# Kernel tuning notes

Hardware: AMD Instinct MI355X
Metric: run time of the kernel (lower is better)

## Reference

```python
import jax, jax.numpy as jnp
import numpy as np

IN_FEATURES = 128
HIDDEN_DIM = 128
ALPHA = 0.2
NEG_INF = -9e15


def setup_inputs() -> dict:
    key = jax.random.key(0)
    k1, k2, k3, k4, k5 = jax.random.split(key, 5)
    N, n_context = 20000, 32
    h_i = jax.random.normal(k1, (N, IN_FEATURES), dtype=jnp.float32)
    context_indices = jax.random.randint(k2, (N, n_context), 0, N, dtype=jnp.int64)
    # learned params (torch nn.Linear default init scale ~ U(-1/sqrt(fan_in), 1/sqrt(fan_in)))
    s1 = 1.0 / np.sqrt(IN_FEATURES)
    s2 = 1.0 / np.sqrt(2 * HIDDEN_DIM)
    W_i = jax.random.uniform(k3, (IN_FEATURES, HIDDEN_DIM), jnp.float32, -s1, s1)
    W_j = jax.random.uniform(k4, (IN_FEATURES, HIDDEN_DIM), jnp.float32, -s1, s1)
    ka, kb = jax.random.split(k5)
    a_w = jax.random.uniform(ka, (2 * HIDDEN_DIM, 1), jnp.float32, -s2, s2)
    a_b = jax.random.uniform(kb, (1,), jnp.float32, -s2, s2)
    return {"h_i": h_i, "context_indices": context_indices,
            "W_i": W_i, "W_j": W_j, "a_w": a_w, "a_b": a_b}


def reference(h_i, context_indices, W_i, W_j, a_w, a_b):
    N, n_context = context_indices.shape
    # -1 padding maps to an extra zero row (torch indexes -1 -> last row of padded table)
    h_padded = jnp.concatenate([h_i, jnp.zeros((1, h_i.shape[1]), h_i.dtype)], axis=0)
    idx = jnp.where(context_indices >= 0, context_indices, N)
    h_j = h_padded[idx]                      # [N, n_context, in_features]
    Wh_i = h_i @ W_i                         # [N, hidden]
    Wh_j = jnp.einsum('ncf,fh->nch', h_j, W_j)  # [N, n_context, hidden]
    # attention_layer(cat(Wh_i, Wh_j)) split into two matvecs (same math as concat)
    a_i, a_j = a_w[:HIDDEN_DIM, 0], a_w[HIDDEN_DIM:, 0]
    e = Wh_i @ a_i                           # [N]
    e = e[:, None] + Wh_j @ a_j + a_b[0]     # [N, n_context]
    e = jax.nn.leaky_relu(e, ALPHA)
    e = jnp.where(context_indices >= 0, e, NEG_INF)
    attn = jax.nn.softmax(e, axis=1)         # [N, n_context]
    h_prime = jnp.einsum('nc,nch->nh', attn, Wh_j)
    return h_prime
```

## Files before the change

kernel.cpp:

```cpp
#include <hip/hip_runtime.h>
#include <hip/hip_fp16.h>

#define GAT_ALPHA 0.2f
#define GAT_NEG_INF -9.0e15f

__global__ void gat_precompute_vi(const float* __restrict__ Wi,
                                  const float* __restrict__ aw,
                                  float* __restrict__ vi) {
    int f = threadIdx.x;
    float s = 0.f;
    #pragma unroll 8
    for (int h = 0; h < 128; ++h)
        s = fmaf(Wi[f * 128 + h], aw[h], s);
    vi[f] = s;
}

__global__ __launch_bounds__(256) void gat_transform(
    const float* __restrict__ h, const float* __restrict__ Wj,
    const float* __restrict__ aw, const float* __restrict__ ab,
    const float* __restrict__ vi,
    __half* __restrict__ Wh16, float* __restrict__ e1, float* __restrict__ e2,
    int N) {
    __shared__ float4 sW[128 * 32];
    const float4* Wj4 = (const float4*)Wj;
    int t = threadIdx.x;
    #pragma unroll
    for (int i = 0; i < 16; ++i) sW[t + i * 256] = Wj4[t + i * 256];
    __syncthreads();

    const int wave = t >> 6, lane = t & 63, half = lane >> 5, l32 = lane & 31;
    const float abv = ab[0];
    const float4 viv = ((const float4*)vi)[l32];
    const float4 ajv = ((const float4*)(aw + 128))[l32];
    const float4* h4 = (const float4*)h;
    const int npairs = (N + 1) >> 1;

    for (int pair = blockIdx.x * 4 + wave; pair < npairs; pair += gridDim.x * 4) {
        int n = 2 * pair + half;
        bool ok = (n < N);
        int nc = ok ? n : 0;
        const float4* hrow = h4 + (size_t)nc * 32;
        float4 hreg = hrow[l32];
        float ax = 0.f, ay = 0.f, az = 0.f, aw4 = 0.f;
        #pragma unroll 4
        for (int fb = 0; fb < 32; ++fb) {
            float4 hq = hrow[fb];
            float4 w0 = sW[(4 * fb + 0) * 32 + l32];
            float4 w1 = sW[(4 * fb + 1) * 32 + l32];
            float4 w2 = sW[(4 * fb + 2) * 32 + l32];
            float4 w3 = sW[(4 * fb + 3) * 32 + l32];
            ax = fmaf(hq.x, w0.x, ax); ay = fmaf(hq.x, w0.y, ay);
            az = fmaf(hq.x, w0.z, az); aw4 = fmaf(hq.x, w0.w, aw4);
            ax = fmaf(hq.y, w1.x, ax); ay = fmaf(hq.y, w1.y, ay);
            az = fmaf(hq.y, w1.z, az); aw4 = fmaf(hq.y, w1.w, aw4);
            ax = fmaf(hq.z, w2.x, ax); ay = fmaf(hq.z, w2.y, ay);
            az = fmaf(hq.z, w2.z, az); aw4 = fmaf(hq.z, w2.w, aw4);
            ax = fmaf(hq.w, w3.x, ax); ay = fmaf(hq.w, w3.y, ay);
            az = fmaf(hq.w, w3.z, az); aw4 = fmaf(hq.w, w3.w, aw4);
        }
        if (ok) {
            union { __half hh[4]; float2 f2; } u;
            u.hh[0] = __float2half(ax); u.hh[1] = __float2half(ay);
            u.hh[2] = __float2half(az); u.hh[3] = __float2half(aw4);
            *(float2*)(Wh16 + (size_t)n * 128 + 4 * l32) = u.f2;
            float pe2 = ax * ajv.x + ay * ajv.y + az * ajv.z + aw4 * ajv.w;
            float pe1 = hreg.x * viv.x + hreg.y * viv.y + hreg.z * viv.z + hreg.w * viv.w;
            #pragma unroll
            for (int mm = 1; mm < 32; mm <<= 1) {
                pe2 += __shfl_xor(pe2, mm);
                pe1 += __shfl_xor(pe1, mm);
            }
            if (l32 == 0) { e2[n] = pe2; e1[n] = pe1 + abv; }
        }
    }
}

__global__ __launch_bounds__(256) void gat_gather(
    const int* __restrict__ ctx, const float* __restrict__ e1,
    const float* __restrict__ e2, const __half* __restrict__ Wh16,
    float* __restrict__ out, int N) {
    int t = threadIdx.x;
    int wave = t >> 6, lane = t & 63, c = lane & 31;
    for (int n = blockIdx.x * 4 + wave; n < N; n += gridDim.x * 4) {
        int iv = ctx[n * 32 + c];
        bool valid = iv >= 0;
        int j = valid ? iv : 0;
        float lg = e1[n] + e2[j];
        lg = fmaxf(lg, GAT_ALPHA * lg);
        lg = valid ? lg : GAT_NEG_INF;
        float m = lg;
        #pragma unroll
        for (int s = 16; s; s >>= 1) m = fmaxf(m, __shfl_xor(m, s));
        float p = valid ? __expf(lg - m) : 0.f;
        float ssum = p;
        #pragma unroll
        for (int s = 16; s; s >>= 1) ssum += __shfl_xor(ssum, s);
        p = (ssum > 0.f) ? p / ssum : 0.f;
        float a0 = 0.f, a1 = 0.f;
        #pragma unroll 16
        for (int cc = 0; cc < 32; ++cc) {
            float w = __shfl(p, cc);
            int jj = __shfl(j, cc);
            __half2 hv = *((const __half2*)(Wh16 + (size_t)jj * 128) + lane);
            float2 f2 = __half22float2(hv);
            a0 = fmaf(w, f2.x, a0);
            a1 = fmaf(w, f2.y, a1);
        }
        ((float2*)(out + (size_t)n * 128))[lane] = make_float2(a0, a1);
    }
}

extern "C" void kernel_launch(void* const* d_in, const int* in_sizes, int n_in,
                              void* d_out, int out_size, void* d_ws, size_t ws_size,
                              hipStream_t stream) {
    const float* h   = (const float*)d_in[0];
    const int*   ctx = (const int*)d_in[1];
    const float* Wi  = (const float*)d_in[2];
    const float* Wj  = (const float*)d_in[3];
    const float* aw  = (const float*)d_in[4];
    const float* ab  = (const float*)d_in[5];
    float* out = (float*)d_out;
    const int N = in_sizes[0] / 128;

    float* vi = (float*)d_ws;
    float* e1 = vi + 256;
    float* e2 = e1 + N;
    __half* Wh16 = (__half*)(e2 + N);

    gat_precompute_vi<<<1, 128, 0, stream>>>(Wi, aw, vi);
    gat_transform<<<512, 256, 0, stream>>>(h, Wj, aw, ab, vi, Wh16, e1, e2, N);
    gat_gather<<<(N + 3) / 4, 256, 0, stream>>>(ctx, e1, e2, Wh16, out, N);
}
```

Before: 110.4 us.

## Use MFMA fp16 for the transform and pack two nodes per wave in gather

The transform kernel is rewritten to run the h·W_j product on 16x16x32 fp16 MFMA instructions, reading a transposed, padded fp16 copy of W_j from shared memory. Each wave now handles 16-row tiles and uses a grid capped at 160 blocks. The gather kernel is rewritten so each wave processes two nodes with 32 lanes each, and each lane loads four halves per neighbour instead of two. The aim is to cut FMA-bound transform time and raise gather efficiency, at the cost of fp16 rounding of inputs and weights in the matmul and scattered 2-byte stores of Wh16.

```diff
diff --git a/kernel.cpp b/kernel.cpp
--- a/kernel.cpp
+++ b/kernel.cpp
@@ -3,6 +3,10 @@
 
 #define GAT_ALPHA 0.2f
 #define GAT_NEG_INF -9.0e15f
+
+typedef _Float16 half8_t __attribute__((ext_vector_type(8)));
+typedef _Float16 half4_t __attribute__((ext_vector_type(4)));
+typedef float f32x4 __attribute__((ext_vector_type(4)));
 
 __global__ void gat_precompute_vi(const float* __restrict__ Wi,
                                   const float* __restrict__ aw,
@@ -15,98 +19,155 @@
     vi[f] = s;
 }
 
-__global__ __launch_bounds__(256) void gat_transform(
+__global__ __launch_bounds__(256) void gat_transform_mfma(
     const float* __restrict__ h, const float* __restrict__ Wj,
     const float* __restrict__ aw, const float* __restrict__ ab,
     const float* __restrict__ vi,
     __half* __restrict__ Wh16, float* __restrict__ e1, float* __restrict__ e2,
     int N) {
-    __shared__ float4 sW[128 * 32];
-    const float4* Wj4 = (const float4*)Wj;
-    int t = threadIdx.x;
-    #pragma unroll
-    for (int i = 0; i < 16; ++i) sW[t + i * 256] = Wj4[t + i * 256];
+    __shared__ _Float16 sWt[128 * 136];
+    const int t = threadIdx.x;
+    for (int i = t; i < 128 * 128; i += 256) {
+        int k = i >> 7, n = i & 127;
+        sWt[n * 136 + k] = (_Float16)Wj[i];
+    }
     __syncthreads();
 
-    const int wave = t >> 6, lane = t & 63, half = lane >> 5, l32 = lane & 31;
+    const int wave = t >> 6, lane = t & 63, q = lane >> 4, l16 = lane & 15;
     const float abv = ab[0];
-    const float4 viv = ((const float4*)vi)[l32];
-    const float4 ajv = ((const float4*)(aw + 128))[l32];
-    const float4* h4 = (const float4*)h;
-    const int npairs = (N + 1) >> 1;
 
-    for (int pair = blockIdx.x * 4 + wave; pair < npairs; pair += gridDim.x * 4) {
-        int n = 2 * pair + half;
-        bool ok = (n < N);
-        int nc = ok ? n : 0;
-        const float4* hrow = h4 + (size_t)nc * 32;
-        float4 hreg = hrow[l32];
-        float ax = 0.f, ay = 0.f, az = 0.f, aw4 = 0.f;
-        #pragma unroll 4
-        for (int fb = 0; fb < 32; ++fb) {
-            float4 hq = hrow[fb];
-            float4 w0 = sW[(4 * fb + 0) * 32 + l32];
-            float4 w1 = sW[(4 * fb + 1) * 32 + l32];
-            float4 w2 = sW[(4 * fb + 2) * 32 + l32];
-            float4 w3 = sW[(4 * fb + 3) * 32 + l32];
-            ax = fmaf(hq.x, w0.x, ax); ay = fmaf(hq.x, w0.y, ay);
-            az = fmaf(hq.x, w0.z, az); aw4 = fmaf(hq.x, w0.w, aw4);
-            ax = fmaf(hq.y, w1.x, ax); ay = fmaf(hq.y, w1.y, ay);
-            az = fmaf(hq.y, w1.z, az); aw4 = fmaf(hq.y, w1.w, aw4);
-            ax = fmaf(hq.z, w2.x, ax); ay = fmaf(hq.z, w2.y, ay);
-            az = fmaf(hq.z, w2.z, az); aw4 = fmaf(hq.z, w2.w, aw4);
-            ax = fmaf(hq.w, w3.x, ax); ay = fmaf(hq.w, w3.y, ay);
-            az = fmaf(hq.w, w3.z, az); aw4 = fmaf(hq.w, w3.w, aw4);
+    float vir[4][8];
+    {
+        const float4* vi4 = (const float4*)vi;
+        #pragma unroll
+        for (int s = 0; s < 4; ++s) {
+            float4 u0 = vi4[s * 8 + q * 2];
+            float4 u1 = vi4[s * 8 + q * 2 + 1];
+            vir[s][0] = u0.x; vir[s][1] = u0.y; vir[s][2] = u0.z; vir[s][3] = u0.w;
+            vir[s][4] = u1.x; vir[s][5] = u1.y; vir[s][6] = u1.z; vir[s][7] = u1.w;
         }
-        if (ok) {
-            union { __half hh[4]; float2 f2; } u;
-            u.hh[0] = __float2half(ax); u.hh[1] = __float2half(ay);
-            u.hh[2] = __float2half(az); u.hh[3] = __float2half(aw4);
-            *(float2*)(Wh16 + (size_t)n * 128 + 4 * l32) = u.f2;
-            float pe2 = ax * ajv.x + ay * ajv.y + az * ajv.z + aw4 * ajv.w;
-            float pe1 = hreg.x * viv.x + hreg.y * viv.y + hreg.z * viv.z + hreg.w * viv.w;
+    }
+    float ajr[8];
+    #pragma unroll
+    for (int c = 0; c < 8; ++c) ajr[c] = aw[128 + c * 16 + l16];
+
+    const int ntiles = (N + 15) >> 4;
+    for (int tile = blockIdx.x * 4 + wave; tile < ntiles; tile += gridDim.x * 4) {
+        const int base = tile << 4;
+        int row = base + l16; if (row >= N) row = N - 1;
+        const float* hp = h + (size_t)row * 128 + q * 8;
+
+        half8_t af[4];
+        float pe1 = 0.f;
+        #pragma unroll
+        for (int s = 0; s < 4; ++s) {
+            float4 f0 = *(const float4*)(hp + s * 32);
+            float4 f1 = *(const float4*)(hp + s * 32 + 4);
+            pe1 = fmaf(f0.x, vir[s][0], pe1); pe1 = fmaf(f0.y, vir[s][1], pe1);
+            pe1 = fmaf(f0.z, vir[s][2], pe1); pe1 = fmaf(f0.w, vir[s][3], pe1);
+            pe1 = fmaf(f1.x, vir[s][4], pe1); pe1 = fmaf(f1.y, vir[s][5], pe1);
+            pe1 = fmaf(f1.z, vir[s][6], pe1); pe1 = fmaf(f1.w, vir[s][7], pe1);
+            half8_t a;
+            a[0] = (_Float16)f0.x; a[1] = (_Float16)f0.y;
+            a[2] = (_Float16)f0.z; a[3] = (_Float16)f0.w;
+            a[4] = (_Float16)f1.x; a[5] = (_Float16)f1.y;
+            a[6] = (_Float16)f1.z; a[7] = (_Float16)f1.w;
+            af[s] = a;
+        }
+
+        f32x4 acc[8];
+        #pragma unroll
+        for (int c = 0; c < 8; ++c) { f32x4 z = {0.f, 0.f, 0.f, 0.f}; acc[c] = z; }
+
+        const _Float16* wbase = sWt + l16 * 136 + q * 8;
+        #pragma unroll
+        for (int s = 0; s < 4; ++s) {
             #pragma unroll
-            for (int mm = 1; mm < 32; mm <<= 1) {
-                pe2 += __shfl_xor(pe2, mm);
-                pe1 += __shfl_xor(pe1, mm);
+            for (int c = 0; c < 8; ++c) {
+                half8_t bf = *(const half8_t*)(wbase + c * (16 * 136) + s * 32);
+                acc[c] = __builtin_amdgcn_mfma_f32_16x16x32_f16(af[s], bf, acc[c], 0, 0, 0);
             }
-            if (l32 == 0) { e2[n] = pe2; e1[n] = pe1 + abv; }
+        }
+
+        const bool full = (base + 16 <= N);
+        float pe2[4] = {0.f, 0.f, 0.f, 0.f};
+        #pragma unroll
+        for (int c = 0; c < 8; ++c) {
+            #pragma unroll
+            for (int r = 0; r < 4; ++r) {
+                float v = acc[c][r];
+                pe2[r] = fmaf(v, ajr[c], pe2[r]);
+                int rr = base + q * 4 + r;
+                if (full || rr < N)
+                    Wh16[(size_t)rr * 128 + (c * 16 + l16)] = __float2half(v);
+            }
+        }
+        #pragma unroll
+        for (int r = 0; r < 4; ++r) {
+            pe2[r] += __shfl_xor(pe2[r], 1);
+            pe2[r] += __shfl_xor(pe2[r], 2);
+            pe2[r] += __shfl_xor(pe2[r], 4);
+            pe2[r] += __shfl_xor(pe2[r], 8);
+        }
+        if (l16 == 0) {
+            #pragma unroll
+            for (int r = 0; r < 4; ++r) {
+                int rr = base + q * 4 + r;
+                if (rr < N) e2[rr] = pe2[r];
+            }
+        }
+        pe1 += __shfl_xor(pe1, 16);
+        pe1 += __shfl_xor(pe1, 32);
+        if (lane < 16) {
+            int rr = base + lane;
+            if (rr < N) e1[rr] = pe1 + abv;
         }
     }
 }
 
-__global__ __launch_bounds__(256) void gat_gather(
+__global__ __launch_bounds__(256) void gat_gather2(
     const int* __restrict__ ctx, const float* __restrict__ e1,
     const float* __restrict__ e2, const __half* __restrict__ Wh16,
     float* __restrict__ out, int N) {
-    int t = threadIdx.x;
-    int wave = t >> 6, lane = t & 63, c = lane & 31;
-    for (int n = blockIdx.x * 4 + wave; n < N; n += gridDim.x * 4) {
-        int iv = ctx[n * 32 + c];
-        bool valid = iv >= 0;
-        int j = valid ? iv : 0;
-        float lg = e1[n] + e2[j];
-        lg = fmaxf(lg, GAT_ALPHA * lg);
-        lg = valid ? lg : GAT_NEG_INF;
-        float m = lg;
-        #pragma unroll
-        for (int s = 16; s; s >>= 1) m = fmaxf(m, __shfl_xor(m, s));
-        float p = valid ? __expf(lg - m) : 0.f;
-        float ssum = p;
-        #pragma unroll
-        for (int s = 16; s; s >>= 1) ssum += __shfl_xor(ssum, s);
-        p = (ssum > 0.f) ? p / ssum : 0.f;
-        float a0 = 0.f, a1 = 0.f;
-        #pragma unroll 16
-        for (int cc = 0; cc < 32; ++cc) {
-            float w = __shfl(p, cc);
-            int jj = __shfl(j, cc);
-            __half2 hv = *((const __half2*)(Wh16 + (size_t)jj * 128) + lane);
-            float2 f2 = __half22float2(hv);
-            a0 = fmaf(w, f2.x, a0);
-            a1 = fmaf(w, f2.y, a1);
-        }
-        ((float2*)(out + (size_t)n * 128))[lane] = make_float2(a0, a1);
+    const int t = threadIdx.x;
+    const int wave = t >> 6, lane = t & 63, hf = lane >> 5, l = lane & 31;
+    const int pair = blockIdx.x * 4 + wave;
+    if (pair * 2 >= N) return;
+    const int n = pair * 2 + hf;
+    const bool okn = (n < N);
+    const int nn = okn ? n : (N - 1);
+
+    const int iv = ctx[(size_t)nn * 32 + l];
+    const bool valid = (iv >= 0);
+    const int j = valid ? iv : 0;
+    float lg = e1[nn] + e2[j];
+    lg = fmaxf(lg, GAT_ALPHA * lg);
+    lg = valid ? lg : GAT_NEG_INF;
+    float m = lg;
+    #pragma unroll
+    for (int s = 16; s; s >>= 1) m = fmaxf(m, __shfl_xor(m, s));
+    float p = valid ? __expf(lg - m) : 0.f;
+    float ss = p;
+    #pragma unroll
+    for (int s = 16; s; s >>= 1) ss += __shfl_xor(ss, s);
+    p = (ss > 0.f) ? p / ss : 0.f;
+
+    const int offB = j << 8;
+    float a0 = 0.f, a1 = 0.f, a2 = 0.f, a3 = 0.f;
+    const char* wb = (const char*)Wh16 + (size_t)(l * 8);
+    #pragma unroll 8
+    for (int cc = 0; cc < 32; ++cc) {
+        int off = __shfl(offB, cc, 32);
+        float w = __shfl(p, cc, 32);
+        half4_t hv = *(const half4_t*)(wb + off);
+        a0 = fmaf(w, (float)hv[0], a0);
+        a1 = fmaf(w, (float)hv[1], a1);
+        a2 = fmaf(w, (float)hv[2], a2);
+        a3 = fmaf(w, (float)hv[3], a3);
+    }
+    if (okn) {
+        float4 o; o.x = a0; o.y = a1; o.z = a2; o.w = a3;
+        ((float4*)(out + (size_t)n * 128))[l] = o;
     }
 }
 
@@ -127,7 +188,11 @@
     float* e2 = e1 + N;
     __half* Wh16 = (__half*)(e2 + N);
 
+    const int ntiles = (N + 15) >> 4;
+    int g1 = (ntiles + 3) / 4; if (g1 > 160) g1 = 160;
+    const int pairs = (N + 1) / 2;
+
     gat_precompute_vi<<<1, 128, 0, stream>>>(Wi, aw, vi);
-    gat_transform<<<512, 256, 0, stream>>>(h, Wj, aw, ab, vi, Wh16, e1, e2, N);
-    gat_gather<<<(N + 3) / 4, 256, 0, stream>>>(ctx, e1, e2, Wh16, out, N);
+    gat_transform_mfma<<<g1, 256, 0, stream>>>(h, Wj, aw, ab, vi, Wh16, e1, e2, N);
+    gat_gather2<<<(pairs + 3) / 4, 256, 0, stream>>>(ctx, e1, e2, Wh16, out, N);
 }
```

After: 102.3 us. -7.4%, faster.
